# Kernel optimization log

Hardware: AMD Instinct MI355X
Metric: run time of the kernel (lower is better)

The kernel has to match this reference:

```python
import jax, jax.numpy as jnp
import numpy as np

THETA = 10000.0

def apply_rope(x, positions):
    # x: [B, H, S, d_k], positions: [S] int
    d_k = x.shape[-1]
    inv_freq = THETA ** (-jnp.arange(0, d_k, 2, dtype=jnp.float32) / d_k)  # [d_k/2]
    ang = positions.astype(jnp.float32)[:, None] * inv_freq[None, :]        # [S, d_k/2]
    cos, sin = jnp.cos(ang), jnp.sin(ang)
    x_even = x[..., 0::2]
    x_odd = x[..., 1::2]
    r_even = x_even * cos - x_odd * sin
    r_odd = x_even * sin + x_odd * cos
    # interleave back
    return jnp.stack([r_even, r_odd], axis=-1).reshape(x.shape)

def setup_inputs() -> dict:
    key = jax.random.key(0)
    k1, k2, k3 = jax.random.split(key, 3)
    B, S, D = 2, 2048, 1024
    x = jax.random.normal(k1, (B, S, D), dtype=jnp.float32)
    token_positions = jnp.arange(S, dtype=jnp.int32)
    W_qkv = jax.random.normal(k2, (3 * D, D), dtype=jnp.float32) * 0.02
    W_o = jax.random.normal(k3, (D, D), dtype=jnp.float32) * 0.02
    return {"x": x, "token_positions": token_positions, "W_qkv": W_qkv, "W_o": W_o}

def reference(x, token_positions, W_qkv, W_o):
    B, S, D = x.shape
    H = 16
    d_k = D // H
    qkv = jnp.einsum('bsd,ed->bse', x, W_qkv)           # [B, S, 3D]
    q, k, v = jnp.split(qkv, 3, axis=-1)
    def to_heads(t):
        return t.reshape(B, S, H, d_k).transpose(0, 2, 1, 3)  # [B, H, S, d_k]
    hq, hk, hv = to_heads(q), to_heads(k), to_heads(v)
    hq = apply_rope(hq, token_positions)
    hk = apply_rope(hk, token_positions)
    scale = d_k ** -0.5
    scores = jnp.einsum('bhqd,bhkd->bhqk', hq, hk) * scale  # [B, H, S, S]
    causal = jnp.tril(jnp.ones((S, S), dtype=bool))
    scores = jnp.where(causal, scores, -jnp.inf)
    attn = jax.nn.softmax(scores, axis=-1)
    out = jnp.einsum('bhqk,bhkd->bhqd', attn, hv)           # [B, H, S, d_k]
    out = out.transpose(0, 2, 1, 3).reshape(B, S, D)
    return jnp.einsum('bsd,ed->bse', out, W_o)
```

## Files before the change

### kernel.cpp

```cpp
#include <hip/hip_runtime.h>
#include <math.h>

typedef short short8 __attribute__((ext_vector_type(8)));
typedef float f32x4 __attribute__((ext_vector_type(4)));

typedef __attribute__((address_space(1))) const void* as1p;
typedef __attribute__((address_space(3))) void* as3p;

__device__ __forceinline__ unsigned short f2bf(float f) {
    unsigned int u = __float_as_uint(f);
    u += 0x7fffu + ((u >> 16) & 1u);
    return (unsigned short)(u >> 16);
}
__device__ __forceinline__ float bf2f(unsigned int bits) {
    return __uint_as_float(bits << 16);
}

__global__ void cvt_all_bf16(const float* __restrict__ x,
                             const float* __restrict__ wqkv,
                             const float* __restrict__ wo,
                             unsigned short* __restrict__ xb,
                             unsigned short* __restrict__ wqkvb,
                             unsigned short* __restrict__ wob) {
    int i = blockIdx.x * blockDim.x + threadIdx.x;
    const float* src;
    unsigned short* dst;
    int off;
    if (i < 1048576)       { src = x;    dst = xb;    off = i; }
    else if (i < 1835008)  { src = wqkv; dst = wqkvb; off = i - 1048576; }
    else                   { src = wo;   dst = wob;   off = i - 1835008; }
    float4 v = ((const float4*)src)[off];
    ushort4 o = make_ushort4(f2bf(v.x), f2bf(v.y), f2bf(v.z), f2bf(v.w));
    ((ushort4*)dst)[off] = o;
}

template <int RF, int NTX, bool BF16_OUT, bool DO_ROPE>
__global__ __launch_bounds__(256) void gemm_nt_mfma(
    const unsigned short* __restrict__ A, const unsigned short* __restrict__ B,
    void* __restrict__ Cv, const int* __restrict__ pos, int N, int K) {
    constexpr int BM = RF * 32;
    __shared__ unsigned short As[BM * 32];
    __shared__ unsigned short Bs[128 * 32];
    const int tid = threadIdx.x;
    const int wave = tid >> 6, lane = tid & 63;
    const int L = blockIdx.x;
    const int xcd = L & 7, idx = L >> 3;
    const int nt_ = xcd * NTX + idx % NTX;
    const int mt  = idx / NTX;
    const int m0 = mt * BM, n0 = nt_ << 7;
    const int wr = ((wave >> 1) & 1) * (RF * 16);
    const int wc = (wave & 1) << 6;

    const int r0 = tid >> 2;
    const int ko = (((tid & 3) ^ ((r0 >> 1) & 3)) << 3);
    const unsigned short* Ap0 = A + (size_t)(m0 + r0) * K + ko;
    const unsigned short* Ap1 = A + (size_t)(m0 + (RF == 4 ? 64 : 0) + r0) * K + ko;
    const unsigned short* Bp0 = B + (size_t)(n0 + r0) * K + ko;
    const unsigned short* Bp1 = B + (size_t)(n0 + 64 + r0) * K + ko;

    f32x4 acc[RF][4] = {};
    const int lro = lane & 15;
    const int cs = ((lane >> 4) ^ ((lro >> 1) & 3)) << 3;

    for (int k0 = 0; k0 < K; k0 += 32) {
        __syncthreads();
        __builtin_amdgcn_global_load_lds((as1p)(Ap0 + k0), (as3p)(As + tid * 8), 16, 0, 0);
        if constexpr (RF == 4)
            __builtin_amdgcn_global_load_lds((as1p)(Ap1 + k0), (as3p)(As + (256 + tid) * 8), 16, 0, 0);
        __builtin_amdgcn_global_load_lds((as1p)(Bp0 + k0), (as3p)(Bs + tid * 8), 16, 0, 0);
        __builtin_amdgcn_global_load_lds((as1p)(Bp1 + k0), (as3p)(Bs + (256 + tid) * 8), 16, 0, 0);
        __syncthreads();

        short8 af[RF], bfr[4];
        #pragma unroll
        for (int i = 0; i < RF; i++) af[i] = *(const short8*)&As[(wr + i * 16 + lro) * 32 + cs];
        #pragma unroll
        for (int j = 0; j < 4; j++) bfr[j] = *(const short8*)&Bs[(wc + j * 16 + lro) * 32 + cs];
        #pragma unroll
        for (int i = 0; i < RF; i++)
            #pragma unroll
            for (int j = 0; j < 4; j++)
                acc[i][j] = __builtin_amdgcn_mfma_f32_16x16x32_bf16(af[i], bfr[j], acc[i][j], 0, 0, 0);
    }

    const int row_b = m0 + wr + ((lane >> 4) << 2);
    const int col_b = n0 + wc + lro;

    if constexpr (DO_ROPE) {
        const int sec = (n0 + wc) >> 10;
        if (sec < 2) {
            const float qs = (sec == 0) ? 0.18033688011112042f : 1.0f;
            const float sgn = (lane & 1) ? 1.0f : -1.0f;
            float ps[RF * 4];
            #pragma unroll
            for (int i = 0; i < RF; i++)
                #pragma unroll
                for (int r = 0; r < 4; r++)
                    ps[i * 4 + r] = (float)pos[(row_b + i * 16 + r) & 2047];
            #pragma unroll
            for (int j = 0; j < 4; j++) {
                float invf_rev = exp2f(-(float)((lro >> 1) + 8 * j) * 0.41524101186092029f)
                                 * 0.15915494309189535f;
                #pragma unroll
                for (int i = 0; i < RF; i++)
                    #pragma unroll
                    for (int r = 0; r < 4; r++) {
                        float rev = ps[i * 4 + r] * invf_rev;
                        rev -= floorf(rev);
                        float c = __builtin_amdgcn_cosf(rev) * qs;
                        float s = __builtin_amdgcn_sinf(rev) * (qs * sgn);
                        float mine = acc[i][j][r];
                        float partner = __shfl_xor(mine, 1, 64);
                        acc[i][j][r] = mine * c + partner * s;
                    }
            }
        }
    }

    #pragma unroll
    for (int i = 0; i < RF; i++)
        #pragma unroll
        for (int j = 0; j < 4; j++)
            #pragma unroll
            for (int r = 0; r < 4; r++) {
                size_t idx2 = (size_t)(row_b + i * 16 + r) * N + (col_b + j * 16);
                if constexpr (BF16_OUT) ((unsigned short*)Cv)[idx2] = f2bf(acc[i][j][r]);
                else ((float*)Cv)[idx2] = acc[i][j][r];
            }
}

__global__ __launch_bounds__(256) void flash_attn_mfma(
    const unsigned short* __restrict__ qkv, unsigned short* __restrict__ Ows) {
    const int S = 2048, D3 = 3072;
    const int L = blockIdx.x + (blockIdx.y << 4) + (blockIdx.z << 8);
    const int xcd = L & 7, t = L >> 3;
    const int pp = t & 15;
    const int g2 = xcd + ((t >> 4) << 3);
    const int h = g2 & 15, b = g2 >> 4;
    const int tid = threadIdx.x, wave = tid >> 6, lane = tid & 63;
    const int lro = lane & 15, grp = lane >> 4;

    __shared__ __align__(16) unsigned short Ks[2][64 * 64];
    __shared__ __align__(16) unsigned int   Vp[2][64 * 36];
    __shared__ __align__(16) unsigned short Ps[64 * 80];

    const int sr = tid >> 3;
    const int sc = ((tid & 7) ^ (sr & 7)) << 3;
    const int kp = tid >> 3, vo = (tid & 7) << 3;
    const int vka = (kp >> 1) + ((kp & 1) << 5);
    const int vcol = (((kp >> 2) ^ (tid & 7)) << 2) | (kp & 3);

    const int cq = grp ^ (lro & 7);
    int kof0[4], kof1[4], vbse[4], vq[4];
    #pragma unroll
    for (int nt = 0; nt < 4; nt++) {
        int R = nt * 16 + lro;
        kof0[nt] = R * 64 + cq * 8;
        kof1[nt] = R * 64 + (cq ^ 4) * 8;
        vbse[nt] = R * 36;
        vq[nt] = (grp ^ (R >> 3)) << 2;
    }
    const int apo = (wave * 16 + lro) * 80 + grp * 8;
    const int prow = wave * 16 + grp * 4;

    const unsigned short* kbg = qkv + (size_t)(b * S) * D3 + 1024 + h * 64;
    const unsigned short* vbg = qkv + (size_t)(b * S) * D3 + 2048 + h * 64;

    for (int ph = 0; ph < 2; ph++) {
        const int qt = ph ? 31 - pp : pp;
        const int q0 = qt << 6;
        const int nkt = qt + 1;

        __syncthreads();
        const unsigned short* qrow =
            qkv + (size_t)(b * S + q0 + wave * 16 + lro) * D3 + h * 64 + grp * 8;
        short8 aq0 = *(const short8*)qrow;
        short8 aq1 = *(const short8*)(qrow + 32);

        __builtin_amdgcn_global_load_lds((as1p)(kbg + (size_t)sr * D3 + sc),
                                         (as3p)&Ks[0][tid * 8], 16, 0, 0);
        __builtin_amdgcn_global_load_lds((as1p)(kbg + (size_t)(sr + 32) * D3 + sc),
                                         (as3p)&Ks[0][(tid + 256) * 8], 16, 0, 0);
        {
            const unsigned short* vs = vbg + (size_t)vka * D3 + vo;
            uint4 va = *(const uint4*)vs;
            uint4 vb = *(const uint4*)(vs + (size_t)16 * D3);
            const unsigned short* pa = (const unsigned short*)&va;
            const unsigned short* pb = (const unsigned short*)&vb;
            #pragma unroll
            for (int j = 0; j < 8; j++)
                Vp[0][(vo + j) * 36 + vcol] = (unsigned)pa[j] | ((unsigned)pb[j] << 16);
        }
        __syncthreads();

        f32x4 acc_o[4] = {};
        float lsum[4] = {0.f, 0.f, 0.f, 0.f};

        for (int kt = 0; kt < nkt; kt++) {
            const int cur = kt & 1, nxt = cur ^ 1;
            const bool pf = (kt + 1 < nkt);
            uint4 va, vb;
            if (pf) {
                const unsigned short* kb1 = kbg + (size_t)((kt + 1) * 64) * D3;
                __builtin_amdgcn_global_load_lds((as1p)(kb1 + (size_t)sr * D3 + sc),
                                                 (as3p)&Ks[nxt][tid * 8], 16, 0, 0);
                __builtin_amdgcn_global_load_lds((as1p)(kb1 + (size_t)(sr + 32) * D3 + sc),
                                                 (as3p)&Ks[nxt][(tid + 256) * 8], 16, 0, 0);
                const unsigned short* vs = vbg + (size_t)((kt + 1) * 64 + vka) * D3 + vo;
                va = *(const uint4*)vs;
                vb = *(const uint4*)(vs + (size_t)16 * D3);
            }

            f32x4 s[4] = {};
            #pragma unroll
            for (int nt = 0; nt < 4; nt++) {
                short8 bk0 = *(const short8*)&Ks[cur][kof0[nt]];
                short8 bk1 = *(const short8*)&Ks[cur][kof1[nt]];
                s[nt] = __builtin_amdgcn_mfma_f32_16x16x32_bf16(aq0, bk0, s[nt], 0, 0, 0);
                s[nt] = __builtin_amdgcn_mfma_f32_16x16x32_bf16(aq1, bk1, s[nt], 0, 0, 0);
            }

            const bool diag = (kt == nkt - 1);
            #pragma unroll
            for (int r = 0; r < 4; r++) {
                float v0 = s[0][r], v1 = s[1][r], v2 = s[2][r], v3 = s[3][r];
                if (diag) {
                    int rowl = prow + r;
                    if (lro > rowl) v0 = -1e30f;
                    if (16 + lro > rowl) v1 = -1e30f;
                    if (32 + lro > rowl) v2 = -1e30f;
                    if (48 + lro > rowl) v3 = -1e30f;
                }
                float p0 = __builtin_amdgcn_exp2f(v0);
                float p1 = __builtin_amdgcn_exp2f(v1);
                float p2 = __builtin_amdgcn_exp2f(v2);
                float p3 = __builtin_amdgcn_exp2f(v3);
                lsum[r] += (p0 + p1) + (p2 + p3);
                unsigned u0 = __float_as_uint(p0) + 0x8000u;
                unsigned u1 = __float_as_uint(p1) + 0x8000u;
                unsigned u2 = __float_as_uint(p2) + 0x8000u;
                unsigned u3 = __float_as_uint(p3) + 0x8000u;
                uint2 w = make_uint2((u0 >> 16) | (u1 & 0xffff0000u),
                                     (u2 >> 16) | (u3 & 0xffff0000u));
                *(uint2*)&Ps[(prow + r) * 80 + lro * 4] = w;
            }

            short8 ap0 = *(const short8*)&Ps[apo];
            short8 ap1 = *(const short8*)&Ps[apo + 32];
            #pragma unroll
            for (int nt = 0; nt < 4; nt++) {
                short8 bv0 = *(const short8*)&Vp[cur][vbse[nt] + vq[nt]];
                short8 bv1 = *(const short8*)&Vp[cur][vbse[nt] + (vq[nt] ^ 16)];
                acc_o[nt] = __builtin_amdgcn_mfma_f32_16x16x32_bf16(ap0, bv0, acc_o[nt], 0, 0, 0);
                acc_o[nt] = __builtin_amdgcn_mfma_f32_16x16x32_bf16(ap1, bv1, acc_o[nt], 0, 0, 0);
            }

            if (pf) {
                const unsigned short* pa = (const unsigned short*)&va;
                const unsigned short* pb = (const unsigned short*)&vb;
                #pragma unroll
                for (int j = 0; j < 8; j++)
                    Vp[nxt][(vo + j) * 36 + vcol] = (unsigned)pa[j] | ((unsigned)pb[j] << 16);
            }
            __syncthreads();
        }

        #pragma unroll
        for (int r = 0; r < 4; r++) {
            float rsum = lsum[r];
            #pragma unroll
            for (int off = 1; off < 16; off <<= 1)
                rsum += __shfl_xor(rsum, off, 16);
            float inv = 1.0f / rsum;
            int row = q0 + prow + r;
            #pragma unroll
            for (int nt = 0; nt < 4; nt++)
                Ows[(size_t)(b * S + row) * 1024 + h * 64 + nt * 16 + lro] =
                    f2bf(acc_o[nt][r] * inv);
        }
    }
}

extern "C" void kernel_launch(void* const* d_in, const int* in_sizes, int n_in,
                              void* d_out, int out_size, void* d_ws, size_t ws_size,
                              hipStream_t stream) {
    const float* x    = (const float*)d_in[0];
    const int*   pos  = (const int*)d_in[1];
    const float* Wqkv = (const float*)d_in[2];
    const float* Wo   = (const float*)d_in[3];
    float* out = (float*)d_out;

    unsigned short* xb    = (unsigned short*)d_ws;
    unsigned short* Wqkvb = xb + (size_t)4096 * 1024;
    unsigned short* Wob   = Wqkvb + (size_t)3072 * 1024;
    unsigned short* qkvb  = Wob + (size_t)1024 * 1024;
    unsigned short* Owsb  = qkvb + (size_t)4096 * 3072;

    cvt_all_bf16<<<8192, 256, 0, stream>>>(x, Wqkv, Wo, xb, Wqkvb, Wob);

    gemm_nt_mfma<4, 3, true, true><<<768, 256, 0, stream>>>(
        xb, Wqkvb, qkvb, pos, 3072, 1024);

    flash_attn_mfma<<<dim3(16, 16, 2), 256, 0, stream>>>(qkvb, Owsb);

    gemm_nt_mfma<2, 1, false, false><<<512, 256, 0, stream>>>(
        Owsb, Wob, out, nullptr, 1024, 1024);
}
```

Before: 186.5 us.

## Split attention key tiles across waves and reduce partial outputs through LDS

Each wave now owns 16 keys of every 64-key tile for all 64 queries, where before each wave owned 16 query rows across all keys. The P tile stays in registers: it is packed to bf16 with v_cvt_pk_bf16_f32 and fed straight into 16x16x16 MFMAs, so the LDS round-trip for P is gone. The cost is a cross-wave reduction of the output accumulators and row sums through LDS at the end of each query tile, plus four times the accumulator registers. The V layout in LDS and the swizzle were also changed to match the new access pattern.

```diff
diff --git a/kernel.cpp b/kernel.cpp
--- a/kernel.cpp
+++ b/kernel.cpp
@@ -3,6 +3,7 @@
 
 typedef short short8 __attribute__((ext_vector_type(8)));
 typedef float f32x4 __attribute__((ext_vector_type(4)));
+typedef unsigned int u32x2 __attribute__((ext_vector_type(2)));
 
 typedef __attribute__((address_space(1))) const void* as1p;
 typedef __attribute__((address_space(3))) void* as3p;
@@ -11,9 +12,6 @@
     unsigned int u = __float_as_uint(f);
     u += 0x7fffu + ((u >> 16) & 1u);
     return (unsigned short)(u >> 16);
-}
-__device__ __forceinline__ float bf2f(unsigned int bits) {
-    return __uint_as_float(bits << 16);
 }
 
 __global__ void cvt_all_bf16(const float* __restrict__ x,
@@ -141,27 +139,20 @@
     const int lro = lane & 15, grp = lane >> 4;
 
     __shared__ __align__(16) unsigned short Ks[2][64 * 64];
-    __shared__ __align__(16) unsigned int   Vp[2][64 * 36];
-    __shared__ __align__(16) unsigned short Ps[64 * 80];
+    __shared__ __align__(16) unsigned int   Vp[2][64 * 34];
+    __shared__ float RedW[4][16][66];
+    __shared__ float Lbuf[4][4][16];
 
     const int sr = tid >> 3;
     const int sc = ((tid & 7) ^ (sr & 7)) << 3;
-    const int kp = tid >> 3, vo = (tid & 7) << 3;
-    const int vka = (kp >> 1) + ((kp & 1) << 5);
-    const int vcol = (((kp >> 2) ^ (tid & 7)) << 2) | (kp & 3);
-
-    const int cq = grp ^ (lro & 7);
-    int kof0[4], kof1[4], vbse[4], vq[4];
-    #pragma unroll
-    for (int nt = 0; nt < 4; nt++) {
-        int R = nt * 16 + lro;
-        kof0[nt] = R * 64 + cq * 8;
-        kof1[nt] = R * 64 + (cq ^ 4) * 8;
-        vbse[nt] = R * 36;
-        vq[nt] = (grp ^ (R >> 3)) << 2;
-    }
-    const int apo = (wave * 16 + lro) * 80 + grp * 8;
-    const int prow = wave * 16 + grp * 4;
+    const int m = tid >> 3;
+    const int vo = (tid & 7) << 3;
+
+    const int Rk = (wave << 4) + lro;
+    const int koffA = Rk * 64 + ((grp ^ (lro & 7)) << 3);
+    const int koffB = Rk * 64 + (((grp ^ 4) ^ (lro & 7)) << 3);
+    const int vcb = (wave << 3) + (grp << 1);
+    const int klb = (wave << 4) + (grp << 2);
 
     const unsigned short* kbg = qkv + (size_t)(b * S) * D3 + 1024 + h * 64;
     const unsigned short* vbg = qkv + (size_t)(b * S) * D3 + 2048 + h * 64;
@@ -172,28 +163,33 @@
         const int nkt = qt + 1;
 
         __syncthreads();
-        const unsigned short* qrow =
-            qkv + (size_t)(b * S + q0 + wave * 16 + lro) * D3 + h * 64 + grp * 8;
-        short8 aq0 = *(const short8*)qrow;
-        short8 aq1 = *(const short8*)(qrow + 32);
+
+        short8 bq[4][2];
+        #pragma unroll
+        for (int f = 0; f < 4; f++) {
+            const unsigned short* qrow =
+                qkv + (size_t)(b * S + q0 + f * 16 + lro) * D3 + h * 64 + grp * 8;
+            bq[f][0] = *(const short8*)qrow;
+            bq[f][1] = *(const short8*)(qrow + 32);
+        }
 
         __builtin_amdgcn_global_load_lds((as1p)(kbg + (size_t)sr * D3 + sc),
                                          (as3p)&Ks[0][tid * 8], 16, 0, 0);
         __builtin_amdgcn_global_load_lds((as1p)(kbg + (size_t)(sr + 32) * D3 + sc),
                                          (as3p)&Ks[0][(tid + 256) * 8], 16, 0, 0);
         {
-            const unsigned short* vs = vbg + (size_t)vka * D3 + vo;
+            const unsigned short* vs = vbg + (size_t)(2 * m) * D3 + vo;
             uint4 va = *(const uint4*)vs;
-            uint4 vb = *(const uint4*)(vs + (size_t)16 * D3);
-            const unsigned short* pa = (const unsigned short*)&va;
-            const unsigned short* pb = (const unsigned short*)&vb;
+            uint4 vb = *(const uint4*)(vs + (size_t)D3);
+            const unsigned short* pa_ = (const unsigned short*)&va;
+            const unsigned short* pb_ = (const unsigned short*)&vb;
             #pragma unroll
             for (int j = 0; j < 8; j++)
-                Vp[0][(vo + j) * 36 + vcol] = (unsigned)pa[j] | ((unsigned)pb[j] << 16);
+                Vp[0][(vo + j) * 34 + m] = (unsigned)pa_[j] | ((unsigned)pb_[j] << 16);
         }
         __syncthreads();
 
-        f32x4 acc_o[4] = {};
+        f32x4 acc[4][4] = {};
         float lsum[4] = {0.f, 0.f, 0.f, 0.f};
 
         for (int kt = 0; kt < nkt; kt++) {
@@ -206,77 +202,115 @@
                                                  (as3p)&Ks[nxt][tid * 8], 16, 0, 0);
                 __builtin_amdgcn_global_load_lds((as1p)(kb1 + (size_t)(sr + 32) * D3 + sc),
                                                  (as3p)&Ks[nxt][(tid + 256) * 8], 16, 0, 0);
-                const unsigned short* vs = vbg + (size_t)((kt + 1) * 64 + vka) * D3 + vo;
+                const unsigned short* vs =
+                    vbg + (size_t)((kt + 1) * 64 + 2 * m) * D3 + vo;
                 va = *(const uint4*)vs;
-                vb = *(const uint4*)(vs + (size_t)16 * D3);
-            }
-
-            f32x4 s[4] = {};
-            #pragma unroll
-            for (int nt = 0; nt < 4; nt++) {
-                short8 bk0 = *(const short8*)&Ks[cur][kof0[nt]];
-                short8 bk1 = *(const short8*)&Ks[cur][kof1[nt]];
-                s[nt] = __builtin_amdgcn_mfma_f32_16x16x32_bf16(aq0, bk0, s[nt], 0, 0, 0);
-                s[nt] = __builtin_amdgcn_mfma_f32_16x16x32_bf16(aq1, bk1, s[nt], 0, 0, 0);
-            }
-
-            const bool diag = (kt == nkt - 1);
-            #pragma unroll
-            for (int r = 0; r < 4; r++) {
-                float v0 = s[0][r], v1 = s[1][r], v2 = s[2][r], v3 = s[3][r];
-                if (diag) {
-                    int rowl = prow + r;
-                    if (lro > rowl) v0 = -1e30f;
-                    if (16 + lro > rowl) v1 = -1e30f;
-                    if (32 + lro > rowl) v2 = -1e30f;
-                    if (48 + lro > rowl) v3 = -1e30f;
+                vb = *(const uint4*)(vs + (size_t)D3);
+            }
+
+            short8 ak0 = *(const short8*)&Ks[cur][koffA];
+            short8 ak1 = *(const short8*)&Ks[cur][koffB];
+            f32x4 s0 = {}, s1 = {}, s2 = {}, s3 = {};
+            s0 = __builtin_amdgcn_mfma_f32_16x16x32_bf16(ak0, bq[0][0], s0, 0, 0, 0);
+            s0 = __builtin_amdgcn_mfma_f32_16x16x32_bf16(ak1, bq[0][1], s0, 0, 0, 0);
+            s1 = __builtin_amdgcn_mfma_f32_16x16x32_bf16(ak0, bq[1][0], s1, 0, 0, 0);
+            s1 = __builtin_amdgcn_mfma_f32_16x16x32_bf16(ak1, bq[1][1], s1, 0, 0, 0);
+            s2 = __builtin_amdgcn_mfma_f32_16x16x32_bf16(ak0, bq[2][0], s2, 0, 0, 0);
+            s2 = __builtin_amdgcn_mfma_f32_16x16x32_bf16(ak1, bq[2][1], s2, 0, 0, 0);
+            s3 = __builtin_amdgcn_mfma_f32_16x16x32_bf16(ak0, bq[3][0], s3, 0, 0, 0);
+            s3 = __builtin_amdgcn_mfma_f32_16x16x32_bf16(ak1, bq[3][1], s3, 0, 0, 0);
+            f32x4 sf[4] = {s0, s1, s2, s3};
+
+            const bool dg = (kt == nkt - 1);
+            u32x2 pw[4];
+            #pragma unroll
+            for (int f = 0; f < 4; f++) {
+                float v0 = sf[f][0], v1 = sf[f][1], v2 = sf[f][2], v3 = sf[f][3];
+                if (dg) {
+                    int thr = (f << 4) + lro - klb;
+                    if (0 > thr) v0 = -1e30f;
+                    if (1 > thr) v1 = -1e30f;
+                    if (2 > thr) v2 = -1e30f;
+                    if (3 > thr) v3 = -1e30f;
                 }
                 float p0 = __builtin_amdgcn_exp2f(v0);
                 float p1 = __builtin_amdgcn_exp2f(v1);
                 float p2 = __builtin_amdgcn_exp2f(v2);
                 float p3 = __builtin_amdgcn_exp2f(v3);
-                lsum[r] += (p0 + p1) + (p2 + p3);
-                unsigned u0 = __float_as_uint(p0) + 0x8000u;
-                unsigned u1 = __float_as_uint(p1) + 0x8000u;
-                unsigned u2 = __float_as_uint(p2) + 0x8000u;
-                unsigned u3 = __float_as_uint(p3) + 0x8000u;
-                uint2 w = make_uint2((u0 >> 16) | (u1 & 0xffff0000u),
-                                     (u2 >> 16) | (u3 & 0xffff0000u));
-                *(uint2*)&Ps[(prow + r) * 80 + lro * 4] = w;
-            }
-
-            short8 ap0 = *(const short8*)&Ps[apo];
-            short8 ap1 = *(const short8*)&Ps[apo + 32];
-            #pragma unroll
-            for (int nt = 0; nt < 4; nt++) {
-                short8 bv0 = *(const short8*)&Vp[cur][vbse[nt] + vq[nt]];
-                short8 bv1 = *(const short8*)&Vp[cur][vbse[nt] + (vq[nt] ^ 16)];
-                acc_o[nt] = __builtin_amdgcn_mfma_f32_16x16x32_bf16(ap0, bv0, acc_o[nt], 0, 0, 0);
-                acc_o[nt] = __builtin_amdgcn_mfma_f32_16x16x32_bf16(ap1, bv1, acc_o[nt], 0, 0, 0);
-            }
+                lsum[f] += (p0 + p1) + (p2 + p3);
+                unsigned u0, u1;
+                asm("v_cvt_pk_bf16_f32 %0, %1, %2" : "=v"(u0) : "v"(p0), "v"(p1));
+                asm("v_cvt_pk_bf16_f32 %0, %1, %2" : "=v"(u1) : "v"(p2), "v"(p3));
+                pw[f][0] = u0;
+                pw[f][1] = u1;
+            }
+
+            u32x2 vv[4];
+            #pragma unroll
+            for (int nt = 0; nt < 4; nt++)
+                vv[nt] = *(const u32x2*)&Vp[cur][(nt * 16 + lro) * 34 + vcb];
+
+            #pragma unroll
+            for (int f = 0; f < 4; f++)
+                #pragma unroll
+                for (int nt = 0; nt < 4; nt++)
+                    asm("v_mfma_f32_16x16x16_bf16 %0, %1, %2, %0"
+                        : "+v"(acc[f][nt]) : "v"(pw[f]), "v"(vv[nt]));
 
             if (pf) {
-                const unsigned short* pa = (const unsigned short*)&va;
-                const unsigned short* pb = (const unsigned short*)&vb;
+                const unsigned short* pa_ = (const unsigned short*)&va;
+                const unsigned short* pb_ = (const unsigned short*)&vb;
                 #pragma unroll
                 for (int j = 0; j < 8; j++)
-                    Vp[nxt][(vo + j) * 36 + vcol] = (unsigned)pa[j] | ((unsigned)pb[j] << 16);
+                    Vp[nxt][(vo + j) * 34 + m] = (unsigned)pa_[j] | ((unsigned)pb_[j] << 16);
             }
             __syncthreads();
         }
 
         #pragma unroll
-        for (int r = 0; r < 4; r++) {
-            float rsum = lsum[r];
-            #pragma unroll
-            for (int off = 1; off < 16; off <<= 1)
-                rsum += __shfl_xor(rsum, off, 16);
-            float inv = 1.0f / rsum;
-            int row = q0 + prow + r;
-            #pragma unroll
-            for (int nt = 0; nt < 4; nt++)
-                Ows[(size_t)(b * S + row) * 1024 + h * 64 + nt * 16 + lro] =
-                    f2bf(acc_o[nt][r] * inv);
+        for (int f = 0; f < 4; f++) {
+            lsum[f] += __shfl_xor(lsum[f], 16, 64);
+            lsum[f] += __shfl_xor(lsum[f], 32, 64);
+        }
+        if (lane < 16) {
+            #pragma unroll
+            for (int f = 0; f < 4; f++) Lbuf[wave][f][lro] = lsum[f];
+        }
+
+        #pragma unroll
+        for (int f = 0; f < 4; f++) {
+            __syncthreads();
+            if (wave != f) {
+                #pragma unroll
+                for (int nt = 0; nt < 4; nt++)
+                    #pragma unroll
+                    for (int r = 0; r < 4; r++)
+                        RedW[wave][(grp << 2) + r][nt * 16 + lro] = acc[f][nt][r];
+            }
+            __syncthreads();
+            if (wave == f) {
+                #pragma unroll
+                for (int w2 = 0; w2 < 4; w2++) {
+                    if (w2 == f) continue;
+                    #pragma unroll
+                    for (int nt = 0; nt < 4; nt++)
+                        #pragma unroll
+                        for (int r = 0; r < 4; r++)
+                            acc[f][nt][r] += RedW[w2][(grp << 2) + r][nt * 16 + lro];
+                }
+                #pragma unroll
+                for (int r = 0; r < 4; r++) {
+                    int q = (grp << 2) + r;
+                    float lt = Lbuf[0][f][q] + Lbuf[1][f][q] +
+                               Lbuf[2][f][q] + Lbuf[3][f][q];
+                    float inv = 1.0f / lt;
+                    int row = q0 + (f << 4) + q;
+                    #pragma unroll
+                    for (int nt = 0; nt < 4; nt++)
+                        Ows[(size_t)(b * S + row) * 1024 + h * 64 + nt * 16 + lro] =
+                            f2bf(acc[f][nt][r] * inv);
+                }
+            }
         }
     }
 }
```

Result: no change. 185.0 us (-0.8%).
